# Kernel tuning notes

Measured on AMD Instinct MI355X. Metric: run time of the kernel, lower is better.

## Reference

```python
import jax, jax.numpy as jnp
import numpy as np
import math

N = 100000
E = 1600000
D = 256          # input_size
H = 64           # head_size = input_size // n_heads = 256 // 4


def setup_inputs() -> dict:
    key = jax.random.key(0)
    k1, k2, k3, k4, k5 = jax.random.split(key, 5)
    X = jax.random.normal(k1, (N, D), dtype=jnp.float32)
    edge_index = jax.random.randint(k2, (2, E), 0, N, dtype=jnp.int64)
    # Linear(input_size, head_size, bias=False) weights, stored as [D, H] so Q = X @ Wq
    s = 1.0 / math.sqrt(D)
    Wq = jax.random.uniform(k3, (D, H), dtype=jnp.float32, minval=-s, maxval=s)
    Wk = jax.random.uniform(k4, (D, H), dtype=jnp.float32, minval=-s, maxval=s)
    Wv = jax.random.uniform(k5, (D, H), dtype=jnp.float32, minval=-s, maxval=s)
    return {"X": X, "Wq": Wq, "Wk": Wk, "Wv": Wv, "edge_index": edge_index}


def reference(X, Wq, Wk, Wv, edge_index):
    dk = math.sqrt(H)
    Q = X @ Wq  # [N, H]
    K = X @ Wk
    V = X @ Wv
    src = edge_index[0]  # row of sparse matrix -> softmax segment (dim=1 softmax)
    dst = edge_index[1]  # column -> neighbor supplying K/V
    scores = jnp.sum(Q[src] * K[dst], axis=-1) / dk  # [E]
    # per-row (per src node) stable softmax over edges
    m = jax.ops.segment_max(scores, src, num_segments=N)          # [N], -inf for empty rows
    m = jnp.where(jnp.isfinite(m), m, 0.0)
    e = jnp.exp(scores - m[src])                                   # [E]
    denom = jax.ops.segment_sum(e, src, num_segments=N)            # [N]
    alpha = e / jnp.maximum(denom[src], 1e-38)                     # [E]
    # scatter-weighted V aggregation: out[i] = sum_{(i,j) in edges} alpha_ij * V[j]
    out = jax.ops.segment_sum(alpha[:, None] * V[dst], src, num_segments=N)  # [N, H]
    return out
```

## Files before the change

kernel.cpp:

```cpp
#include <hip/hip_runtime.h>

typedef unsigned short u16;
typedef unsigned int u32;
typedef short short8 __attribute__((ext_vector_type(8)));
typedef float f32x4 __attribute__((ext_vector_type(4)));
typedef u32 u32x4 __attribute__((ext_vector_type(4)));

__device__ __forceinline__ u16 f2bf(float f) {
    union { float f; u32 i; } c; c.f = f;
    u32 i = c.i;
    return (u16)((i + 0x7FFFu + ((i >> 16) & 1u)) >> 16);
}
__device__ __forceinline__ float bf2f(u16 u) {
    union { u32 i; float f; } c; c.i = ((u32)u) << 16; return c.f;
}
__device__ __forceinline__ void bf2x(u32 p, float& lo, float& hi) {
    union { u32 i; float f; } a, b;
    a.i = p << 16; b.i = p & 0xFFFF0000u;
    lo = a.f; hi = b.f;
}
__device__ __forceinline__ u32 cvtpk_bf16(float lo, float hi) {
    u32 r;
    asm("v_cvt_pk_bf16_f32 %0, %1, %2" : "=v"(r) : "v"(lo), "v"(hi));
    return r;
}

__global__ void wfrag_kernel(const float* __restrict__ Wq,
                             const float* __restrict__ Wk,
                             const float* __restrict__ Wv,
                             u16* __restrict__ wf)
{
    int idx = blockIdx.x * 256 + threadIdx.x;
    if (idx >= 12 * 8 * 64) return;
    int lane = idx & 63;
    int s = (idx >> 6) & 7;
    int t = idx >> 9;
    int n = t * 16 + (lane & 15);
    const float* Wsrc = (n < 64) ? Wq : ((n < 128) ? Wk : Wv);
    int col = n & 63;
    int kbase = s * 32 + (lane >> 4) * 8;
    u16 o[8];
#pragma unroll
    for (int j = 0; j < 8; ++j) o[j] = f2bf(Wsrc[(size_t)(kbase + j) * 64 + col]);
    *(short8*)(wf + (size_t)idx * 8) = *(const short8*)o;
}

#define TM 32
__global__ __launch_bounds__(256, 2) void qkv_mfma(
    const float* __restrict__ X, const u16* __restrict__ wf,
    float* __restrict__ Qs, u16* __restrict__ KVsb,
    int N, int NT)
{
    __shared__ float xs[TM * 256];

    const int tid  = threadIdx.x;
    const int lane = tid & 63;
    const int wave = tid >> 6;
    const int m    = lane & 15;
    const int quad = lane >> 4;
    const int t0   = wave * 3;

    const short8* wfp = (const short8*)wf;
    short8 bfr0[8], bfr1[8], bfr2[8];
#pragma unroll
    for (int s = 0; s < 8; ++s) {
        bfr0[s] = wfp[(size_t)((t0 + 0) * 8 + s) * 64 + lane];
        bfr1[s] = wfp[(size_t)((t0 + 1) * 8 + s) * 64 + lane];
        bfr2[s] = wfp[(size_t)((t0 + 2) * 8 + s) * 64 + lane];
    }

    for (int tile = blockIdx.x; tile < NT; tile += gridDim.x) {
#pragma unroll
        for (int it = 0; it < 8; ++it) {
            int c0  = (it * 4 + wave) * 64;
            int c   = c0 + lane;
            int row = c >> 6;
            int sblk = (c & 63) ^ (row & 7);
            int arow = tile * TM + row;
            if (arow >= N) arow = N - 1;
            const float* g = X + (size_t)arow * 256 + sblk * 4;
            float* l = xs + c0 * 4;
            __builtin_amdgcn_global_load_lds(
                (const __attribute__((address_space(1))) void*)g,
                (__attribute__((address_space(3))) void*)l, 16, 0, 0);
        }
        __syncthreads();

        f32x4 acc[2][3];
#pragma unroll
        for (int rb = 0; rb < 2; ++rb)
#pragma unroll
            for (int tt = 0; tt < 3; ++tt) acc[rb][tt] = (f32x4)0.f;

#pragma unroll
        for (int rb = 0; rb < 2; ++rb) {
            const int row = rb * 16 + m;
            const float* xrow = xs + row * 256;
            const int sw = m & 7;
#pragma unroll
            for (int s = 0; s < 8; ++s) {
                int B0 = quad * 2 + s * 8;
                float4 a0 = *(const float4*)(xrow + ((B0)     ^ sw) * 4);
                float4 a1 = *(const float4*)(xrow + ((B0 + 1) ^ sw) * 4);
                union { u32x4 u; short8 s8; } af;
                af.u.x = cvtpk_bf16(a0.x, a0.y);
                af.u.y = cvtpk_bf16(a0.z, a0.w);
                af.u.z = cvtpk_bf16(a1.x, a1.y);
                af.u.w = cvtpk_bf16(a1.z, a1.w);
                acc[rb][0] = __builtin_amdgcn_mfma_f32_16x16x32_bf16(af.s8, bfr0[s], acc[rb][0], 0, 0, 0);
                acc[rb][1] = __builtin_amdgcn_mfma_f32_16x16x32_bf16(af.s8, bfr1[s], acc[rb][1], 0, 0, 0);
                acc[rb][2] = __builtin_amdgcn_mfma_f32_16x16x32_bf16(af.s8, bfr2[s], acc[rb][2], 0, 0, 0);
            }
        }

#pragma unroll
        for (int rb = 0; rb < 2; ++rb) {
            int rbase = tile * TM + rb * 16 + quad * 4;
#pragma unroll
            for (int tt = 0; tt < 3; ++tt) {
                int t = t0 + tt;
                int col = (t & 3) * 16 + m;
#pragma unroll
                for (int r = 0; r < 4; ++r) {
                    int rr = rbase + r;
                    if (rr >= N) continue;
                    float v = acc[rb][tt][r];
                    if (t < 4)      Qs  [(size_t)rr * 64  + col]      = v;
                    else if (t < 8) KVsb[(size_t)rr * 128 + col]      = f2bf(v);
                    else            KVsb[(size_t)rr * 128 + 64 + col] = f2bf(v);
                }
            }
        }
        __syncthreads();
    }
}


#define CB 320

__global__ __launch_bounds__(256) void count_kernel(
    const int* __restrict__ src, int* __restrict__ bcnt,
    int E, int N, int NB, int chunk)
{
    __shared__ int cnt[512];
    for (int i = threadIdx.x; i < 512; i += 256) cnt[i] = 0;
    __syncthreads();
    int lo = blockIdx.x * chunk;
    int hi = min(E, lo + chunk);
    for (int e = lo + (int)threadIdx.x; e < hi; e += 256) {
        int s = src[e];
        if ((unsigned)s < (unsigned)N) atomicAdd(&cnt[s >> 8], 1);
    }
    __syncthreads();
    int* row = bcnt + (size_t)blockIdx.x * NB;
    for (int b = threadIdx.x; b < NB; b += 256) row[b] = cnt[b];
}

__global__ __launch_bounds__(512) void scan_kernel(
    const int* __restrict__ bcnt, int* __restrict__ blockbase,
    int* __restrict__ bbase, int* __restrict__ row_ptr_N, int NB)
{
    __shared__ int sd[512];
    int t = threadIdx.x;
    int run = 0;
    if (t < NB) {
        for (int blk = 0; blk < CB; ++blk) {
            int v = bcnt[(size_t)blk * NB + t];
            blockbase[(size_t)blk * NB + t] = run;
            run += v;
        }
    }
    sd[t] = (t < NB) ? run : 0;
    __syncthreads();
    for (int off = 1; off < 512; off <<= 1) {
        int x = (t >= off) ? sd[t - off] : 0;
        __syncthreads();
        sd[t] += x;
        __syncthreads();
    }
    if (t < NB) {
        bbase[t] = sd[t] - run;
        if (t == NB - 1) {
            bbase[NB] = sd[t];
            *row_ptr_N = sd[t];
        }
    }
}

__global__ __launch_bounds__(256) void scatter_pairs_kernel(
    const int* __restrict__ src, const int* __restrict__ dst,
    const int* __restrict__ bbase, const int* __restrict__ blockbase,
    u32* __restrict__ pairs, int E, int N, int NB, int chunk)
{
    __shared__ int cnt[512];
    __shared__ int basei[512];
    for (int i = threadIdx.x; i < 512; i += 256) cnt[i] = 0;
    __syncthreads();
    int lo = blockIdx.x * chunk;
    int hi = min(E, lo + chunk);
    for (int e = lo + (int)threadIdx.x; e < hi; e += 256) {
        int s = src[e];
        if ((unsigned)s < (unsigned)N) atomicAdd(&cnt[s >> 8], 1);
    }
    __syncthreads();
    const int* bb = blockbase + (size_t)blockIdx.x * NB;
    for (int b = threadIdx.x; b < NB; b += 256)
        basei[b] = bbase[b] + bb[b];
    __syncthreads();
    for (int i = threadIdx.x; i < 512; i += 256) cnt[i] = 0;
    __syncthreads();
    for (int e = lo + (int)threadIdx.x; e < hi; e += 256) {
        int s = src[e];
        if ((unsigned)s >= (unsigned)N) continue;
        int d = dst[e];
        if ((unsigned)d >= (unsigned)N) d = 0;
        int bk = s >> 8;
        int p = basei[bk] + atomicAdd(&cnt[bk], 1);
        pairs[p] = (u32)d | ((u32)(s & 255) << 24);
    }
}

#define MAXB 6144
__global__ __launch_bounds__(256) void sort_bucket_kernel(
    const u32* __restrict__ pairs, const int* __restrict__ bbase,
    int* __restrict__ row_ptr, int* __restrict__ sorted_dst, int N)
{
    __shared__ int deg[256];
    __shared__ int off[256];
    __shared__ int cur[256];
    __shared__ int ldst[MAXB];

    int bk = blockIdx.x;
    int n0 = bk * 256;
    int nn = min(256, N - n0);
    int base = bbase[bk];
    int size = bbase[bk + 1] - base;
    int t = threadIdx.x;

    deg[t] = 0;
    __syncthreads();
    for (int i = t; i < size; i += 256)
        atomicAdd(&deg[pairs[base + i] >> 24], 1);
    __syncthreads();
    off[t] = deg[t];
    __syncthreads();
    for (int s = 1; s < 256; s <<= 1) {
        int x = (t >= s) ? off[t - s] : 0;
        __syncthreads();
        off[t] += x;
        __syncthreads();
    }
    int excl = off[t] - deg[t];
    cur[t] = excl;
    if (t < nn) row_ptr[n0 + t] = base + excl;
    __syncthreads();
    int cap = min(size, MAXB);
    for (int i = t; i < size; i += 256) {
        u32 pr = pairs[base + i];
        int p = atomicAdd(&cur[pr >> 24], 1);
        if (p < MAXB) ldst[p] = (int)(pr & 0xFFFFFFu);
    }
    __syncthreads();
    for (int i = t; i < cap; i += 256)
        sorted_dst[base + i] = ldst[i];
    for (int i = cap + t; i < size; i += 256)
        sorted_dst[base + i] = 0;
}

__global__ __launch_bounds__(256) void attn_csr(
    const float* __restrict__ Qs, const u16* __restrict__ KVsb,
    const int* __restrict__ row_ptr, const int* __restrict__ sdst,
    float* __restrict__ out, int N)
{
    int sg = (int)((blockIdx.x * 256 + threadIdx.x) >> 3);
    if (sg >= N) return;
    int sl = threadIdx.x & 7;

    const float* qp = Qs + (size_t)sg * 64 + sl * 8;
    float4 q0 = *(const float4*)(qp);
    float4 q1 = *(const float4*)(qp + 4);

    int beg = row_ptr[sg];
    int end = row_ptr[sg + 1];

    float l = 0.f;
    float a0 = 0.f, a1 = 0.f, a2 = 0.f, a3 = 0.f;
    float a4 = 0.f, a5 = 0.f, a6 = 0.f, a7 = 0.f;

    if (beg < end) {
        const int last = end - 1;
        uint4 kr[8], vr[8];
        int pd[8];

#pragma unroll
        for (int i = 0; i < 8; ++i) {
            int e = beg + i;
            int d = sdst[e <= last ? e : last];
            const u16* kv = KVsb + (size_t)d * 128 + sl * 8;
            kr[i] = *(const uint4*)(kv);
            vr[i] = *(const uint4*)(kv + 64);
            int ep = beg + 8 + i;
            pd[i] = sdst[ep <= last ? ep : last];
        }

        for (int base = beg; base < end; base += 8) {
#pragma unroll
            for (int i = 0; i < 8; ++i) {
                int e = base + i;
                uint4 k = kr[i], v = vr[i];

                {
                    const u16* kv = KVsb + (size_t)pd[i] * 128 + sl * 8;
                    kr[i] = *(const uint4*)(kv);
                    vr[i] = *(const uint4*)(kv + 64);
                    int ep = e + 16;
                    pd[i] = sdst[ep <= last ? ep : last];
                }

                float k0, k1, k2, k3, k4, k5, k6, k7;
                bf2x(k.x, k0, k1); bf2x(k.y, k2, k3);
                bf2x(k.z, k4, k5); bf2x(k.w, k6, k7);

                float p = q0.x * k0 + q0.y * k1 + q0.z * k2 + q0.w * k3
                        + q1.x * k4 + q1.y * k5 + q1.z * k6 + q1.w * k7;
                p += __shfl_xor(p, 1);
                p += __shfl_xor(p, 2);
                p += __shfl_xor(p, 4);

                float pe = __expf(p * 0.125f);

                float v0, v1, v2, v3, v4, v5, v6, v7;
                bf2x(v.x, v0, v1); bf2x(v.y, v2, v3);
                bf2x(v.z, v4, v5); bf2x(v.w, v6, v7);

                if (e < end) {
                    l += pe;
                    a0 += pe * v0; a1 += pe * v1; a2 += pe * v2; a3 += pe * v3;
                    a4 += pe * v4; a5 += pe * v5; a6 += pe * v6; a7 += pe * v7;
                }
            }
        }
    }

    float inv = (l > 0.f) ? (1.f / l) : 0.f;
    float* op = out + (size_t)sg * 64 + sl * 8;
    *(float4*)(op)     = make_float4(a0 * inv, a1 * inv, a2 * inv, a3 * inv);
    *(float4*)(op + 4) = make_float4(a4 * inv, a5 * inv, a6 * inv, a7 * inv);
}

extern "C" void kernel_launch(void* const* d_in, const int* in_sizes, int n_in,
                              void* d_out, int out_size, void* d_ws, size_t ws_size,
                              hipStream_t stream)
{
    const float* X  = (const float*)d_in[0];
    const float* Wq = (const float*)d_in[1];
    const float* Wk = (const float*)d_in[2];
    const float* Wv = (const float*)d_in[3];
    const int*   ei = (const int*)d_in[4];

    const int N = in_sizes[0] / 256;
    const int E = in_sizes[4] / 2;
    const int* src = ei;
    const int* dst = ei + E;
    const int NB = (N + 255) >> 8;

    char* w = (char*)d_ws;
    float* Qs = (float*)w;      w += (size_t)N * 64 * sizeof(float);
    u16* KVsb = (u16*)w;        w += (size_t)N * 128 * sizeof(u16);
    u32* pairs = (u32*)w;       w += (size_t)E * sizeof(u32);
    int* sorted_dst = (int*)w;  w += (size_t)E * sizeof(int);
    int* row_ptr = (int*)w;     w += (size_t)(N + 1) * sizeof(int);
    int* bbase = (int*)w;       w += (size_t)(NB + 1) * sizeof(int);
    int* bcnt = (int*)w;        w += (size_t)CB * NB * sizeof(int);
    int* blockbase = (int*)w;   w += (size_t)CB * NB * sizeof(int);
    u16* wf = (u16*)w;          w += (size_t)12 * 8 * 64 * 8 * sizeof(u16);

    const int chunk = (E + CB - 1) / CB;
    const int NT = (N + TM - 1) / TM;

    wfrag_kernel<<<24, 256, 0, stream>>>(Wq, Wk, Wv, wf);
    qkv_mfma<<<768, 256, 0, stream>>>(X, wf, Qs, KVsb, N, NT);

    count_kernel<<<CB, 256, 0, stream>>>(src, bcnt, E, N, NB, chunk);
    scan_kernel<<<1, 512, 0, stream>>>(bcnt, blockbase, bbase, row_ptr + N, NB);
    scatter_pairs_kernel<<<CB, 256, 0, stream>>>(
        src, dst, bbase, blockbase, pairs, E, N, NB, chunk);
    sort_bucket_kernel<<<NB, 256, 0, stream>>>(pairs, bbase, row_ptr, sorted_dst, N);

    attn_csr<<<(N * 8 + 255) / 256, 256, 0, stream>>>(
        Qs, KVsb, row_ptr, sorted_dst, (float*)d_out, N);
}
```

Before: 324.7 us.

## Parallelize bucket scan, shrink attention prefetch depth, split attention launch

Replaces the single-block serial scan over 320 count rows with a two-level scan: one block per bucket scans its transposed per-block counts, then a single block scans the bucket totals. The count/blockbase arrays are transposed to bucket-major to suit this. The attention kernel's software prefetch depth drops from 8 to 4 edges, which lowers register pressure, and the attention launch is split into two halves over node ranges. This adds one kernel launch and reduces the memory-latency hiding per wave in the gather loop.

```diff
diff --git a/kernel.cpp b/kernel.cpp
--- a/kernel.cpp
+++ b/kernel.cpp
@@ -152,25 +152,38 @@
         if ((unsigned)s < (unsigned)N) atomicAdd(&cnt[s >> 8], 1);
     }
     __syncthreads();
-    int* row = bcnt + (size_t)blockIdx.x * NB;
-    for (int b = threadIdx.x; b < NB; b += 256) row[b] = cnt[b];
-}
-
-__global__ __launch_bounds__(512) void scan_kernel(
+    for (int b = threadIdx.x; b < NB; b += 256)
+        bcnt[(size_t)b * CB + blockIdx.x] = cnt[b];
+}
+
+__global__ __launch_bounds__(512) void scanB1_kernel(
     const int* __restrict__ bcnt, int* __restrict__ blockbase,
-    int* __restrict__ bbase, int* __restrict__ row_ptr_N, int NB)
+    int* __restrict__ colsum, int NB)
+{
+    __shared__ int sd[512];
+    int b = blockIdx.x;
+    int t = threadIdx.x;
+    int v = (t < CB) ? bcnt[(size_t)b * CB + t] : 0;
+    sd[t] = v;
+    __syncthreads();
+    for (int off = 1; off < 512; off <<= 1) {
+        int x = (t >= off) ? sd[t - off] : 0;
+        __syncthreads();
+        sd[t] += x;
+        __syncthreads();
+    }
+    if (t < CB) blockbase[(size_t)b * CB + t] = sd[t] - v;
+    if (t == 511) colsum[b] = sd[511];
+}
+
+__global__ __launch_bounds__(512) void scanB2_kernel(
+    const int* __restrict__ colsum, int* __restrict__ bbase,
+    int* __restrict__ row_ptr_N, int NB)
 {
     __shared__ int sd[512];
     int t = threadIdx.x;
-    int run = 0;
-    if (t < NB) {
-        for (int blk = 0; blk < CB; ++blk) {
-            int v = bcnt[(size_t)blk * NB + t];
-            blockbase[(size_t)blk * NB + t] = run;
-            run += v;
-        }
-    }
-    sd[t] = (t < NB) ? run : 0;
+    int v = (t < NB) ? colsum[t] : 0;
+    sd[t] = v;
     __syncthreads();
     for (int off = 1; off < 512; off <<= 1) {
         int x = (t >= off) ? sd[t - off] : 0;
@@ -179,7 +192,7 @@
         __syncthreads();
     }
     if (t < NB) {
-        bbase[t] = sd[t] - run;
+        bbase[t] = sd[t] - v;
         if (t == NB - 1) {
             bbase[NB] = sd[t];
             *row_ptr_N = sd[t];
@@ -203,9 +216,8 @@
         if ((unsigned)s < (unsigned)N) atomicAdd(&cnt[s >> 8], 1);
     }
     __syncthreads();
-    const int* bb = blockbase + (size_t)blockIdx.x * NB;
     for (int b = threadIdx.x; b < NB; b += 256)
-        basei[b] = bbase[b] + bb[b];
+        basei[b] = bbase[b] + blockbase[(size_t)b * CB + blockIdx.x];
     __syncthreads();
     for (int i = threadIdx.x; i < 512; i += 256) cnt[i] = 0;
     __syncthreads();
@@ -270,10 +282,10 @@
 __global__ __launch_bounds__(256) void attn_csr(
     const float* __restrict__ Qs, const u16* __restrict__ KVsb,
     const int* __restrict__ row_ptr, const int* __restrict__ sdst,
-    float* __restrict__ out, int N)
-{
-    int sg = (int)((blockIdx.x * 256 + threadIdx.x) >> 3);
-    if (sg >= N) return;
+    float* __restrict__ out, int n0, int n1)
+{
+    int sg = n0 + (int)((blockIdx.x * 256 + threadIdx.x) >> 3);
+    if (sg >= n1) return;
     int sl = threadIdx.x & 7;
 
     const float* qp = Qs + (size_t)sg * 64 + sl * 8;
@@ -289,23 +301,23 @@
 
     if (beg < end) {
         const int last = end - 1;
-        uint4 kr[8], vr[8];
-        int pd[8];
-
-#pragma unroll
-        for (int i = 0; i < 8; ++i) {
+        uint4 kr[4], vr[4];
+        int pd[4];
+
+#pragma unroll
+        for (int i = 0; i < 4; ++i) {
             int e = beg + i;
             int d = sdst[e <= last ? e : last];
             const u16* kv = KVsb + (size_t)d * 128 + sl * 8;
             kr[i] = *(const uint4*)(kv);
             vr[i] = *(const uint4*)(kv + 64);
-            int ep = beg + 8 + i;
+            int ep = beg + 4 + i;
             pd[i] = sdst[ep <= last ? ep : last];
         }
 
-        for (int base = beg; base < end; base += 8) {
-#pragma unroll
-            for (int i = 0; i < 8; ++i) {
+        for (int base = beg; base < end; base += 4) {
+#pragma unroll
+            for (int i = 0; i < 4; ++i) {
                 int e = base + i;
                 uint4 k = kr[i], v = vr[i];
 
@@ -313,7 +325,7 @@
                     const u16* kv = KVsb + (size_t)pd[i] * 128 + sl * 8;
                     kr[i] = *(const uint4*)(kv);
                     vr[i] = *(const uint4*)(kv + 64);
-                    int ep = e + 16;
+                    int ep = e + 8;
                     pd[i] = sdst[ep <= last ? ep : last];
                 }
 
@@ -371,8 +383,9 @@
     int* sorted_dst = (int*)w;  w += (size_t)E * sizeof(int);
     int* row_ptr = (int*)w;     w += (size_t)(N + 1) * sizeof(int);
     int* bbase = (int*)w;       w += (size_t)(NB + 1) * sizeof(int);
-    int* bcnt = (int*)w;        w += (size_t)CB * NB * sizeof(int);
-    int* blockbase = (int*)w;   w += (size_t)CB * NB * sizeof(int);
+    int* bcnt = (int*)w;        w += (size_t)NB * CB * sizeof(int);
+    int* blockbase = (int*)w;   w += (size_t)NB * CB * sizeof(int);
+    int* colsum = (int*)w;      w += (size_t)(NB + 1) * sizeof(int);
     u16* wf = (u16*)w;          w += (size_t)12 * 8 * 64 * 8 * sizeof(u16);
 
     const int chunk = (E + CB - 1) / CB;
@@ -382,11 +395,15 @@
     qkv_mfma<<<768, 256, 0, stream>>>(X, wf, Qs, KVsb, N, NT);
 
     count_kernel<<<CB, 256, 0, stream>>>(src, bcnt, E, N, NB, chunk);
-    scan_kernel<<<1, 512, 0, stream>>>(bcnt, blockbase, bbase, row_ptr + N, NB);
+    scanB1_kernel<<<NB, 512, 0, stream>>>(bcnt, blockbase, colsum, NB);
+    scanB2_kernel<<<1, 512, 0, stream>>>(colsum, bbase, row_ptr + N, NB);
     scatter_pairs_kernel<<<CB, 256, 0, stream>>>(
         src, dst, bbase, blockbase, pairs, E, N, NB, chunk);
     sort_bucket_kernel<<<NB, 256, 0, stream>>>(pairs, bbase, row_ptr, sorted_dst, N);
 
-    attn_csr<<<(N * 8 + 255) / 256, 256, 0, stream>>>(
-        Qs, KVsb, row_ptr, sorted_dst, (float*)d_out, N);
-}
+    const int Nh = N / 2;
+    attn_csr<<<(Nh * 8 + 255) / 256, 256, 0, stream>>>(
+        Qs, KVsb, row_ptr, sorted_dst, (float*)d_out, 0, Nh);
+    attn_csr<<<((N - Nh) * 8 + 255) / 256, 256, 0, stream>>>(
+        Qs, KVsb, row_ptr, sorted_dst, (float*)d_out, Nh, N);
+}
```

New measurement: 310.8 us. 4.3% less time.
